# Kernel optimization log

Measured on AMD Instinct MI355X. Metric: run time of the kernel, lower is better.

## Reference

```python
import jax, jax.numpy as jnp
import numpy as np
import math

D_INPUT = 1024
D_Q = 1024
D_K = 1024
D_V = 1024
D_MODEL = 1024
B, S = 4, 2048


def setup_inputs() -> dict:
    key = jax.random.key(0)
    ks = jax.random.split(key, 9)
    sc = 0.02
    return {
        "x": jax.random.normal(ks[0], (B, S, D_INPUT), dtype=jnp.float32),
        "wq": jax.random.normal(ks[1], (D_INPUT, D_Q), dtype=jnp.float32) * sc,
        "bq": jnp.zeros((D_Q,), dtype=jnp.float32),
        "wk": jax.random.normal(ks[2], (D_INPUT, D_K), dtype=jnp.float32) * sc,
        "bk": jnp.zeros((D_K,), dtype=jnp.float32),
        "wv": jax.random.normal(ks[3], (D_INPUT, D_V), dtype=jnp.float32) * sc,
        "bv": jnp.zeros((D_V,), dtype=jnp.float32),
        "wp": jax.random.normal(ks[4], (D_V, D_MODEL), dtype=jnp.float32) * sc,
        "bp": jnp.zeros((D_MODEL,), dtype=jnp.float32),
    }


def reference(x, wq, bq, wk, bk, wv, bv, wp, bp):
    scale = math.sqrt(D_K)  # NOTE: original MULTIPLIES by sqrt(d_k)
    q = x @ wq + bq  # [B,S,Dq]
    k = x @ wk + bk  # [B,S,Dk]
    v = x @ wv + bv  # [B,S,Dv]
    scores = jnp.einsum('bsd,btd->bst', q, k) * scale
    p_attn = jax.nn.softmax(scores, axis=-1)
    # dropout: inference mode (training=False) -> identity
    context = jnp.einsum('bst,btd->bsd', p_attn, v)
    output = context @ wp + bp
    return (output, p_attn)
```

## Files before the change

kernel.cpp:

```cpp
#include <hip/hip_runtime.h>

typedef unsigned short u16;
typedef short bf16x8 __attribute__((ext_vector_type(8)));
typedef float floatx4 __attribute__((ext_vector_type(4)));

static __device__ __forceinline__ u16 f2bf(float f) {
  unsigned int u = __float_as_uint(f);
  unsigned int lsb = (u >> 16) & 1u;
  u += 0x7FFFu + lsb;
  return (u16)(u >> 16);
}
static __device__ __forceinline__ float bf2f(u16 u) {
  return __uint_as_float(((unsigned int)u) << 16);
}

static __device__ __forceinline__ void gl_lds16(const u16* g, u16* l) {
  __builtin_amdgcn_global_load_lds(
      (const __attribute__((address_space(1))) void*)g,
      (__attribute__((address_space(3))) void*)l, 16, 0, 0);
}

__global__ __launch_bounds__(256)
void prep_all(const float* __restrict__ wq, const float* __restrict__ wk,
              const float* __restrict__ wv, const float* __restrict__ wp,
              const float* __restrict__ bq, const float* __restrict__ bk,
              const float* __restrict__ x,
              u16* __restrict__ qkThi, u16* __restrict__ qkTlo,
              u16* __restrict__ wvThi, u16* __restrict__ wpThi,
              float* __restrict__ bqk,
              u16* __restrict__ xhi, u16* __restrict__ xlo,
              u16* __restrict__ xThi) {
  __shared__ float t[32][33];
  const int z = blockIdx.z;
  const int tid = threadIdx.x;
  const int lr = tid >> 3;
  const int lc = (tid & 7) * 4;

  if (z == 4) {
    if (blockIdx.y == 0 && blockIdx.x < 8) {
      const int i = blockIdx.x * 256 + tid;
      bqk[i] = (i < 1024) ? bq[i] : bk[i - 1024];
    }
    return;
  }

  if (z >= 5) {
    const int r0 = ((z - 5) * 32 + blockIdx.y) * 32;
    const int c0 = blockIdx.x * 32;
    float4 v = *(const float4*)(x + (size_t)(r0 + lr) * 1024 + c0 + lc);
    float f[4] = {v.x, v.y, v.z, v.w};
    t[lr][lc + 0] = v.x; t[lr][lc + 1] = v.y; t[lr][lc + 2] = v.z; t[lr][lc + 3] = v.w;
    u16 ph[4], pl[4];
#pragma unroll
    for (int j = 0; j < 4; j++) {
      ph[j] = f2bf(f[j]);
      pl[j] = f2bf(f[j] - bf2f(ph[j]));
    }
    const size_t o = (size_t)(r0 + lr) * 1024 + c0 + lc;
    *(uint2*)(xhi + o) = *(uint2*)ph;
    *(uint2*)(xlo + o) = *(uint2*)pl;
    __syncthreads();
    u16 pt[4];
#pragma unroll
    for (int j = 0; j < 4; j++) pt[j] = f2bf(t[lc + j][lr]);
    const int b = r0 >> 11, rt = r0 & 2047;
    *(uint2*)(xThi + (size_t)b * (1024 * 2048) + (size_t)(c0 + lr) * 2048 + rt + lc) =
        *(uint2*)pt;
    return;
  }

  const float* in = (z == 0) ? wq : (z == 1) ? wk : (z == 2) ? wv : wp;
  u16* hi = (z == 2) ? wvThi : (z == 3) ? wpThi : (qkThi + (size_t)z * 1024 * 1024);
  u16* lo = (z == 0) ? qkTlo : (z == 1) ? (qkTlo + 1024 * 1024) : (u16*)nullptr;
  const int want_lo = (z < 2);

  const int r0 = blockIdx.y * 32, c0 = blockIdx.x * 32;
  float4 v = *(const float4*)(in + (size_t)(r0 + lr) * 1024 + c0 + lc);
  t[lr][lc + 0] = v.x; t[lr][lc + 1] = v.y; t[lr][lc + 2] = v.z; t[lr][lc + 3] = v.w;
  __syncthreads();
  u16 ph[4], pl[4];
#pragma unroll
  for (int j = 0; j < 4; j++) {
    float f = t[lc + j][lr];
    ph[j] = f2bf(f);
    if (want_lo) pl[j] = f2bf(f - bf2f(ph[j]));
  }
  const size_t o = (size_t)(c0 + lr) * 1024 + r0 + lc;
  *(uint2*)(hi + o) = *(uint2*)ph;
  if (want_lo) *(uint2*)(lo + o) = *(uint2*)pl;
}

template<int BM, int SPLIT, int OM, int HB>
__global__ __launch_bounds__(512, 2)
void gemm8(const u16* __restrict__ Ahi, const u16* __restrict__ Alo,
           const u16* __restrict__ Bhi, const u16* __restrict__ Blo,
           const float* __restrict__ bias,
           void* __restrict__ C0, void* __restrict__ C1,
           void* __restrict__ C2, void* __restrict__ C3,
           int lda, int ldb, int ldc, int NP,
           long long aB, long long bB, long long cB, float scale) {
  constexpr int AF = BM / 32;
  constexpr int ASLOT = BM * 32;
  constexpr int L = 2 + BM / 128;
  __shared__ __align__(16) u16 As[4 * ASLOT];
  __shared__ __align__(16) u16 Bs[4 * 8192];

  const int gx = gridDim.x, gy = gridDim.y, gz = gridDim.z;
  const int flat = blockIdx.x + gx * (blockIdx.y + gy * blockIdx.z);
  const int nwg = gx * gy * gz;
  const int lg = (flat & 7) * (nwg >> 3) + (flat >> 3);
  const int bx = lg % gx;
  const int by = (lg / gx) % gy;
  const int bz = lg / (gx * gy);

  const int m0 = by * BM, n0 = bx * 256;
  const u16* pAhi = Ahi + (size_t)bz * aB;
  const u16* pAlo = SPLIT ? (Alo + (size_t)bz * aB) : (const u16*)nullptr;
  const u16* pBhi = Bhi + (size_t)bz * bB;
  const u16* pBlo = SPLIT ? (Blo + (size_t)bz * bB) : (const u16*)nullptr;

  const int tid = threadIdx.x;
  const int w = tid >> 6;
  const int L64 = tid & 63;
  const int rr = L64 & 15, quad = L64 >> 4;
  const int wm = (w >> 2) * (BM / 2);
  const int wn = (w & 3) * 64;

  const int rbase = w * 16 + (L64 >> 2);
  const int coff = (((L64 & 3) ^ ((L64 >> 3) & 3)) << 3);
  const size_t arow = (size_t)(m0 + rbase) * lda + coff;
  const size_t brow = (size_t)(n0 + rbase) * ldb + coff;
  u16* const ldA = As + w * 512;
  u16* const ldB = Bs + w * 512;

  const int aoff = ((wm + rr) << 5) + ((quad ^ ((rr >> 1) & 3)) << 3);
  const int boff = ((wn + rr) << 5) + ((quad ^ ((rr >> 1) & 3)) << 3);

  auto stageA = [&](int H) {
    const u16* src;
    int koff;
    if (SPLIT) {
      const int kt = H >> 1;
      src = (kt < 32) ? pAhi : pAlo;
      koff = ((kt & 15) << 6) + ((H & 1) << 5);
    } else {
      src = pAhi;
      koff = H << 5;
    }
    const u16* g = src + arow + koff;
    u16* l = ldA + (H & 3) * ASLOT;
    gl_lds16(g, l);
    if (BM == 256) gl_lds16(g + (size_t)128 * lda, l + 4096);
  };
  auto stageB = [&](int H) {
    const u16* src;
    int koff;
    if (SPLIT) {
      const int kt = H >> 1;
      src = (kt < 16) ? pBhi : (kt < 32) ? pBlo : pBhi;
      koff = ((kt & 15) << 6) + ((H & 1) << 5);
    } else {
      src = pBhi;
      koff = H << 5;
    }
    const u16* g = src + brow + koff;
    u16* l = ldB + (H & 3) * 8192;
    gl_lds16(g, l);
    gl_lds16(g + (size_t)128 * ldb, l + 4096);
  };

  floatx4 acc[AF][4] = {};
  bf16x8 aE[AF], aO[AF], b01E[2], b01O[2], b23[2];

#define RD_SET(slot, A_, B_)                                                   \
  {                                                                            \
    const u16* ab_ = As + ((slot) & 3) * ASLOT + aoff;                         \
    const u16* bb_ = Bs + ((slot) & 3) * 8192 + boff;                          \
    _Pragma("unroll")                                                          \
    for (int i = 0; i < AF; i++) A_[i] = *(const bf16x8*)(ab_ + i * 512);      \
    B_[0] = *(const bf16x8*)(bb_);                                             \
    B_[1] = *(const bf16x8*)(bb_ + 512);                                       \
  }

#define PAIRX(H, AC, B01C, AN, B01N, STG, RDN, VM)                             \
  {                                                                            \
    __builtin_amdgcn_sched_barrier(0);                                         \
                                                        \
    {                                                                          \
      const u16* bb_ = Bs + ((H) & 3) * 8192 + boff;                           \
      b23[0] = *(const bf16x8*)(bb_ + 1024);                                   \
      b23[1] = *(const bf16x8*)(bb_ + 1536);                                   \
    }                                                                          \
    __builtin_amdgcn_sched_barrier(0);                                         \
                                                            \
    __builtin_amdgcn_s_setprio(1);                                             \
    _Pragma("unroll")                                                          \
    for (int i = 0; i < AF; i++) {                                             \
      acc[i][0] = __builtin_amdgcn_mfma_f32_16x16x32_bf16(AC[i], B01C[0], acc[i][0], 0, 0, 0); \
      acc[i][1] = __builtin_amdgcn_mfma_f32_16x16x32_bf16(AC[i], B01C[1], acc[i][1], 0, 0, 0); \
    }                                                                          \
    __builtin_amdgcn_s_setprio(0);                                             \
    __builtin_amdgcn_sched_barrier(0);                                         \
                               \
    if ((VM) == 4) asm volatile("s_waitcnt vmcnt(4)");                         \
    else if ((VM) == 3) asm volatile("s_waitcnt vmcnt(3)");                    \
    else if ((VM) == 0) asm volatile("s_waitcnt vmcnt(0)");                    \
    __builtin_amdgcn_s_barrier();                                              \
                                \
    if (RDN) RD_SET((H) + 1, AN, B01N);                                        \
    if (STG) { stageA((H) + 3); stageB((H) + 3); }                             \
    __builtin_amdgcn_sched_barrier(0);                                         \
                                                            \
    __builtin_amdgcn_s_setprio(1);                                             \
    _Pragma("unroll")                                                          \
    for (int i = 0; i < AF; i++) {                                             \
      acc[i][2] = __builtin_amdgcn_mfma_f32_16x16x32_bf16(AC[i], b23[0], acc[i][2], 0, 0, 0); \
      acc[i][3] = __builtin_amdgcn_mfma_f32_16x16x32_bf16(AC[i], b23[1], acc[i][3], 0, 0, 0); \
    }                                                                          \
    __builtin_amdgcn_s_setprio(0);                                             \
  }

  stageA(0); stageB(0); stageA(1); stageB(1); stageA(2); stageB(2);
  if (L == 4) asm volatile("s_waitcnt vmcnt(8)");
  else        asm volatile("s_waitcnt vmcnt(6)");
  __builtin_amdgcn_s_barrier();
  RD_SET(0, aE, b01E);

  for (int H = 0; H + 4 < NP; H += 2) {
    PAIRX(H,     aE, b01E, aO, b01O, true, true, L);
    PAIRX(H + 1, aO, b01O, aE, b01E, true, true, L);
  }
  {
    const int T = NP - 4;
    PAIRX(T,     aE, b01E, aO, b01O, true,  true,  L);
    PAIRX(T + 1, aO, b01O, aE, b01E, false, true,  L);
    PAIRX(T + 2, aE, b01E, aO, b01O, false, true,  0);
    PAIRX(T + 3, aO, b01O, aE, b01E, false, false, -1);
  }
#undef PAIRX
#undef RD_SET

#pragma unroll
  for (int i = 0; i < AF; i++) {
    const int mb = m0 + wm + i * 16 + quad * 4;
#pragma unroll
    for (int j = 0; j < 4; j++) {
      const int col = n0 + wn + j * 16 + rr;
      float bvs = 0.f;
      if (HB) bvs = bias[col];
      if (OM == 5) {
        u16* hi; u16* lo;
        if (col < 1024) { hi = (u16*)C0; lo = (u16*)C1; }
        else            { hi = (u16*)C2; lo = (u16*)C3; }
        const int cc = col & 1023;
#pragma unroll
        for (int ii = 0; ii < 4; ii++) {
          const float v = acc[i][j][ii] + bvs;
          const size_t idx = (size_t)(mb + ii) * 1024 + cc;
          const u16 h = f2bf(v);
          hi[idx] = h;
          lo[idx] = f2bf(v - bf2f(h));
        }
      } else if (OM == 0) {
        u16* Cb = (u16*)C0 + (size_t)bz * cB;
#pragma unroll
        for (int ii = 0; ii < 4; ii++) {
          const float v = acc[i][j][ii] * scale + bvs;
          Cb[(size_t)(mb + ii) * ldc + col] = f2bf(v);
        }
      } else {
        float* Cf = (float*)C0 + (size_t)bz * cB;
#pragma unroll
        for (int ii = 0; ii < 4; ii++)
          Cf[(size_t)(mb + ii) * ldc + col] = acc[i][j][ii] * scale + bvs;
      }
    }
  }
}

__global__ __launch_bounds__(256)
void softmax_rows(float* __restrict__ S, u16* __restrict__ Pb) {
  const int row = blockIdx.x;
  float* s = S + (size_t)row * 2048;
  const int tid = threadIdx.x;
  const int w = tid >> 6;
  __shared__ float redm[4];
  __shared__ float reds[4];

  float v[8];
  float mx = -1e30f;
#pragma unroll
  for (int i = 0; i < 8; i++) {
    v[i] = s[tid + 256 * i];
    mx = fmaxf(mx, v[i]);
  }
#pragma unroll
  for (int o = 32; o > 0; o >>= 1) mx = fmaxf(mx, __shfl_xor(mx, o, 64));
  if ((tid & 63) == 0) redm[w] = mx;
  __syncthreads();
  mx = fmaxf(fmaxf(redm[0], redm[1]), fmaxf(redm[2], redm[3]));

  float sum = 0.f;
#pragma unroll
  for (int i = 0; i < 8; i++) {
    v[i] = __expf(v[i] - mx);
    sum += v[i];
  }
#pragma unroll
  for (int o = 32; o > 0; o >>= 1) sum += __shfl_xor(sum, o, 64);
  if ((tid & 63) == 0) reds[w] = sum;
  __syncthreads();
  sum = reds[0] + reds[1] + reds[2] + reds[3];
  const float rs = 1.0f / sum;
#pragma unroll
  for (int i = 0; i < 8; i++) {
    const float p = v[i] * rs;
    s[tid + 256 * i] = p;
    Pb[(size_t)row * 2048 + tid + 256 * i] = f2bf(p);
  }
}

extern "C" void kernel_launch(void* const* d_in, const int* in_sizes, int n_in,
                              void* d_out, int out_size, void* d_ws, size_t ws_size,
                              hipStream_t stream) {
  const float* x  = (const float*)d_in[0];
  const float* wq = (const float*)d_in[1];
  const float* bq = (const float*)d_in[2];
  const float* wk = (const float*)d_in[3];
  const float* bk = (const float*)d_in[4];
  const float* wv = (const float*)d_in[5];
  const float* bv = (const float*)d_in[6];
  const float* wp = (const float*)d_in[7];
  const float* bp = (const float*)d_in[8];

  const size_t MB = 1024 * 1024;
  char* ws = (char*)d_ws;
  u16* qkThi = (u16*)(ws + 0 * MB);
  u16* qkTlo = (u16*)(ws + 4 * MB);
  u16* wvThi = (u16*)(ws + 8 * MB);
  u16* wpThi = (u16*)(ws + 10 * MB);
  float* bqk = (float*)(ws + 12 * MB);
  u16* xhi   = (u16*)(ws + 13 * MB);
  u16* xlo   = (u16*)(ws + 29 * MB);
  u16* qhi   = (u16*)(ws + 45 * MB);
  u16* qlo   = (u16*)(ws + 61 * MB);
  u16* khi   = (u16*)(ws + 77 * MB);
  u16* klo   = (u16*)(ws + 93 * MB);
  u16* xThi  = (u16*)(ws + 109 * MB);
  u16* pbf   = khi;
  u16* px    = qhi;
  u16* ctx   = qlo;

  float* outp = (float*)d_out;
  float* scf  = (float*)d_out + 8388608;

  prep_all<<<dim3(32, 32, 13), dim3(256), 0, stream>>>(
      wq, wk, wv, wp, bq, bk, x, qkThi, qkTlo, wvThi, wpThi, bqk, xhi, xlo, xThi);

  gemm8<256, 1, 5, 1><<<dim3(8, 32, 1), dim3(512), 0, stream>>>(
      xhi, xlo, qkThi, qkTlo, bqk, qhi, qlo, khi, klo,
      1024, 1024, 1024, 96, 0, 0, 0, 1.0f);

  gemm8<256, 1, 2, 0><<<dim3(8, 8, 4), dim3(512), 0, stream>>>(
      qhi, qlo, khi, klo, nullptr, scf, nullptr, nullptr, nullptr,
      1024, 1024, 2048, 96, 2048LL * 1024, 2048LL * 1024, 2048LL * 2048, 32.0f);

  softmax_rows<<<dim3(8192), dim3(256), 0, stream>>>(scf, pbf);

  gemm8<128, 0, 0, 0><<<dim3(4, 16, 4), dim3(512), 0, stream>>>(
      pbf, nullptr, xThi, nullptr, nullptr, px, nullptr, nullptr, nullptr,
      2048, 2048, 1024, 64, 2048LL * 2048, 1024LL * 2048, 2048LL * 1024, 1.0f);

  gemm8<128, 0, 0, 1><<<dim3(4, 64, 1), dim3(512), 0, stream>>>(
      px, nullptr, wvThi, nullptr, bv, ctx, nullptr, nullptr, nullptr,
      1024, 1024, 1024, 32, 0, 0, 0, 1.0f);

  gemm8<128, 0, 2, 1><<<dim3(4, 64, 1), dim3(512), 0, stream>>>(
      ctx, nullptr, wpThi, nullptr, bp, outp, nullptr, nullptr, nullptr,
      1024, 1024, 1024, 32, 0, 0, 0, 1.0f);
}
```

Baseline: 458.8 us.

## Fix GEMM tile at 128x256 with triple-buffered LDS and single register set

Removes the BM template so every GEMM uses a 128-row tile, including the split-bf16 QK projection and score GEMMs that previously used 256 rows. LDS staging goes from 4 slots to 3 (modulo-3 indexing), fragment registers drop from even/odd double sets to a single set, and launch bounds rise to 4 blocks per CU. The aim is higher occupancy and lower LDS use. In exchange, the large GEMMs reuse less data per tile and the next fragments are read after the MFMAs rather than overlapped with them.

```diff
diff --git a/kernel.cpp b/kernel.cpp
--- a/kernel.cpp
+++ b/kernel.cpp
@@ -90,8 +90,8 @@
   if (want_lo) *(uint2*)(lo + o) = *(uint2*)pl;
 }
 
-template<int BM, int SPLIT, int OM, int HB>
-__global__ __launch_bounds__(512, 2)
+template<int SPLIT, int OM, int HB>
+__global__ __launch_bounds__(512, 4)
 void gemm8(const u16* __restrict__ Ahi, const u16* __restrict__ Alo,
            const u16* __restrict__ Bhi, const u16* __restrict__ Blo,
            const float* __restrict__ bias,
@@ -99,11 +99,8 @@
            void* __restrict__ C2, void* __restrict__ C3,
            int lda, int ldb, int ldc, int NP,
            long long aB, long long bB, long long cB, float scale) {
-  constexpr int AF = BM / 32;
-  constexpr int ASLOT = BM * 32;
-  constexpr int L = 2 + BM / 128;
-  __shared__ __align__(16) u16 As[4 * ASLOT];
-  __shared__ __align__(16) u16 Bs[4 * 8192];
+  __shared__ __align__(16) u16 As[3 * 4096];
+  __shared__ __align__(16) u16 Bs[3 * 8192];
 
   const int gx = gridDim.x, gy = gridDim.y, gz = gridDim.z;
   const int flat = blockIdx.x + gx * (blockIdx.y + gy * blockIdx.z);
@@ -113,7 +110,7 @@
   const int by = (lg / gx) % gy;
   const int bz = lg / (gx * gy);
 
-  const int m0 = by * BM, n0 = bx * 256;
+  const int m0 = by * 128, n0 = bx * 256;
   const u16* pAhi = Ahi + (size_t)bz * aB;
   const u16* pAlo = SPLIT ? (Alo + (size_t)bz * aB) : (const u16*)nullptr;
   const u16* pBhi = Bhi + (size_t)bz * bB;
@@ -123,7 +120,7 @@
   const int w = tid >> 6;
   const int L64 = tid & 63;
   const int rr = L64 & 15, quad = L64 >> 4;
-  const int wm = (w >> 2) * (BM / 2);
+  const int wm = (w >> 2) * 64;
   const int wn = (w & 3) * 64;
 
   const int rbase = w * 16 + (L64 >> 2);
@@ -147,10 +144,7 @@
       src = pAhi;
       koff = H << 5;
     }
-    const u16* g = src + arow + koff;
-    u16* l = ldA + (H & 3) * ASLOT;
-    gl_lds16(g, l);
-    if (BM == 256) gl_lds16(g + (size_t)128 * lda, l + 4096);
+    gl_lds16(src + arow + koff, ldA + (H % 3) * 4096);
   };
   auto stageB = [&](int H) {
     const u16* src;
@@ -164,30 +158,20 @@
       koff = H << 5;
     }
     const u16* g = src + brow + koff;
-    u16* l = ldB + (H & 3) * 8192;
+    u16* l = ldB + (H % 3) * 8192;
     gl_lds16(g, l);
     gl_lds16(g + (size_t)128 * ldb, l + 4096);
   };
 
-  floatx4 acc[AF][4] = {};
-  bf16x8 aE[AF], aO[AF], b01E[2], b01O[2], b23[2];
-
-#define RD_SET(slot, A_, B_)                                                   \
-  {                                                                            \
-    const u16* ab_ = As + ((slot) & 3) * ASLOT + aoff;                         \
-    const u16* bb_ = Bs + ((slot) & 3) * 8192 + boff;                          \
-    _Pragma("unroll")                                                          \
-    for (int i = 0; i < AF; i++) A_[i] = *(const bf16x8*)(ab_ + i * 512);      \
-    B_[0] = *(const bf16x8*)(bb_);                                             \
-    B_[1] = *(const bf16x8*)(bb_ + 512);                                       \
-  }
-
-#define PAIRX(H, AC, B01C, AN, B01N, STG, RDN, VM)                             \
+  floatx4 acc[4][4] = {};
+  bf16x8 a[4], b01[2], b23[2];
+
+#define PAIRX(H, STG, RDN, VM)                                                 \
   {                                                                            \
     __builtin_amdgcn_sched_barrier(0);                                         \
                                                         \
     {                                                                          \
-      const u16* bb_ = Bs + ((H) & 3) * 8192 + boff;                           \
+      const u16* bb_ = Bs + ((H) % 3) * 8192 + boff;                           \
       b23[0] = *(const bf16x8*)(bb_ + 1024);                                   \
       b23[1] = *(const bf16x8*)(bb_ + 1536);                                   \
     }                                                                          \
@@ -195,53 +179,70 @@
                                                             \
     __builtin_amdgcn_s_setprio(1);                                             \
     _Pragma("unroll")                                                          \
-    for (int i = 0; i < AF; i++) {                                             \
-      acc[i][0] = __builtin_amdgcn_mfma_f32_16x16x32_bf16(AC[i], B01C[0], acc[i][0], 0, 0, 0); \
-      acc[i][1] = __builtin_amdgcn_mfma_f32_16x16x32_bf16(AC[i], B01C[1], acc[i][1], 0, 0, 0); \
+    for (int i = 0; i < 4; i++) {                                              \
+      acc[i][0] = __builtin_amdgcn_mfma_f32_16x16x32_bf16(a[i], b01[0], acc[i][0], 0, 0, 0); \
+      acc[i][1] = __builtin_amdgcn_mfma_f32_16x16x32_bf16(a[i], b01[1], acc[i][1], 0, 0, 0); \
     }                                                                          \
     __builtin_amdgcn_s_setprio(0);                                             \
     __builtin_amdgcn_sched_barrier(0);                                         \
-                               \
-    if ((VM) == 4) asm volatile("s_waitcnt vmcnt(4)");                         \
-    else if ((VM) == 3) asm volatile("s_waitcnt vmcnt(3)");                    \
-    else if ((VM) == 0) asm volatile("s_waitcnt vmcnt(0)");                    \
+                             \
+    asm volatile("s_waitcnt lgkmcnt(0)" ::: "memory");                         \
     __builtin_amdgcn_s_barrier();                                              \
-                                \
-    if (RDN) RD_SET((H) + 1, AN, B01N);                                        \
+    __builtin_amdgcn_sched_barrier(0);                                         \
+                                       \
     if (STG) { stageA((H) + 3); stageB((H) + 3); }                             \
+    __builtin_amdgcn_sched_barrier(0);                                         \
+                          \
+    if ((VM) == 6) asm volatile("s_waitcnt vmcnt(6)" ::: "memory");            \
+    else if ((VM) == 3) asm volatile("s_waitcnt vmcnt(3)" ::: "memory");       \
+    else if ((VM) == 0) asm volatile("s_waitcnt vmcnt(0)" ::: "memory");       \
+    __builtin_amdgcn_sched_barrier(0);                                         \
+                       \
+    if (RDN) {                                                                 \
+      const u16* bb_ = Bs + (((H) + 1) % 3) * 8192 + boff;                     \
+      b01[0] = *(const bf16x8*)(bb_);                                          \
+      b01[1] = *(const bf16x8*)(bb_ + 512);                                    \
+    }                                                                          \
     __builtin_amdgcn_sched_barrier(0);                                         \
                                                             \
     __builtin_amdgcn_s_setprio(1);                                             \
     _Pragma("unroll")                                                          \
-    for (int i = 0; i < AF; i++) {                                             \
-      acc[i][2] = __builtin_amdgcn_mfma_f32_16x16x32_bf16(AC[i], b23[0], acc[i][2], 0, 0, 0); \
-      acc[i][3] = __builtin_amdgcn_mfma_f32_16x16x32_bf16(AC[i], b23[1], acc[i][3], 0, 0, 0); \
+    for (int i = 0; i < 4; i++) {                                              \
+      acc[i][2] = __builtin_amdgcn_mfma_f32_16x16x32_bf16(a[i], b23[0], acc[i][2], 0, 0, 0); \
+      acc[i][3] = __builtin_amdgcn_mfma_f32_16x16x32_bf16(a[i], b23[1], acc[i][3], 0, 0, 0); \
     }                                                                          \
     __builtin_amdgcn_s_setprio(0);                                             \
+    __builtin_amdgcn_sched_barrier(0);                                         \
+                           \
+    if (RDN) {                                                                 \
+      const u16* ab_ = As + (((H) + 1) % 3) * 4096 + aoff;                     \
+      _Pragma("unroll")                                                        \
+      for (int i = 0; i < 4; i++) a[i] = *(const bf16x8*)(ab_ + i * 512);      \
+    }                                                                          \
   }
 
   stageA(0); stageB(0); stageA(1); stageB(1); stageA(2); stageB(2);
-  if (L == 4) asm volatile("s_waitcnt vmcnt(8)");
-  else        asm volatile("s_waitcnt vmcnt(6)");
+  asm volatile("s_waitcnt vmcnt(6)" ::: "memory");
   __builtin_amdgcn_s_barrier();
-  RD_SET(0, aE, b01E);
-
-  for (int H = 0; H + 4 < NP; H += 2) {
-    PAIRX(H,     aE, b01E, aO, b01O, true, true, L);
-    PAIRX(H + 1, aO, b01O, aE, b01E, true, true, L);
-  }
+  __builtin_amdgcn_sched_barrier(0);
   {
-    const int T = NP - 4;
-    PAIRX(T,     aE, b01E, aO, b01O, true,  true,  L);
-    PAIRX(T + 1, aO, b01O, aE, b01E, false, true,  L);
-    PAIRX(T + 2, aE, b01E, aO, b01O, false, true,  0);
-    PAIRX(T + 3, aO, b01O, aE, b01E, false, false, -1);
-  }
+    const u16* bb_ = Bs + boff;
+    b01[0] = *(const bf16x8*)(bb_);
+    b01[1] = *(const bf16x8*)(bb_ + 512);
+    const u16* ab_ = As + aoff;
+#pragma unroll
+    for (int i = 0; i < 4; i++) a[i] = *(const bf16x8*)(ab_ + i * 512);
+  }
+
+  for (int H = 0; H <= NP - 4; ++H)
+    PAIRX(H, true, true, 6);
+  PAIRX(NP - 3, false, true, 3);
+  PAIRX(NP - 2, false, true, 0);
+  PAIRX(NP - 1, false, false, -1);
 #undef PAIRX
-#undef RD_SET
-
-#pragma unroll
-  for (int i = 0; i < AF; i++) {
+
+#pragma unroll
+  for (int i = 0; i < 4; i++) {
     const int mb = m0 + wm + i * 16 + quad * 4;
 #pragma unroll
     for (int j = 0; j < 4; j++) {
@@ -357,25 +358,25 @@
   prep_all<<<dim3(32, 32, 13), dim3(256), 0, stream>>>(
       wq, wk, wv, wp, bq, bk, x, qkThi, qkTlo, wvThi, wpThi, bqk, xhi, xlo, xThi);
 
-  gemm8<256, 1, 5, 1><<<dim3(8, 32, 1), dim3(512), 0, stream>>>(
+  gemm8<1, 5, 1><<<dim3(8, 64, 1), dim3(512), 0, stream>>>(
       xhi, xlo, qkThi, qkTlo, bqk, qhi, qlo, khi, klo,
       1024, 1024, 1024, 96, 0, 0, 0, 1.0f);
 
-  gemm8<256, 1, 2, 0><<<dim3(8, 8, 4), dim3(512), 0, stream>>>(
+  gemm8<1, 2, 0><<<dim3(8, 16, 4), dim3(512), 0, stream>>>(
       qhi, qlo, khi, klo, nullptr, scf, nullptr, nullptr, nullptr,
       1024, 1024, 2048, 96, 2048LL * 1024, 2048LL * 1024, 2048LL * 2048, 32.0f);
 
   softmax_rows<<<dim3(8192), dim3(256), 0, stream>>>(scf, pbf);
 
-  gemm8<128, 0, 0, 0><<<dim3(4, 16, 4), dim3(512), 0, stream>>>(
+  gemm8<0, 0, 0><<<dim3(4, 16, 4), dim3(512), 0, stream>>>(
       pbf, nullptr, xThi, nullptr, nullptr, px, nullptr, nullptr, nullptr,
       2048, 2048, 1024, 64, 2048LL * 2048, 1024LL * 2048, 2048LL * 1024, 1.0f);
 
-  gemm8<128, 0, 0, 1><<<dim3(4, 64, 1), dim3(512), 0, stream>>>(
+  gemm8<0, 0, 1><<<dim3(4, 64, 1), dim3(512), 0, stream>>>(
       px, nullptr, wvThi, nullptr, bv, ctx, nullptr, nullptr, nullptr,
       1024, 1024, 1024, 32, 0, 0, 0, 1.0f);
 
-  gemm8<128, 0, 2, 1><<<dim3(4, 64, 1), dim3(512), 0, stream>>>(
+  gemm8<0, 2, 1><<<dim3(4, 64, 1), dim3(512), 0, stream>>>(
       ctx, nullptr, wpThi, nullptr, bp, outp, nullptr, nullptr, nullptr,
       1024, 1024, 1024, 32, 0, 0, 0, 1.0f);
 }
```

After: 502.4 us. +9.5%, slower.

## Restructure GEMM main loop with asymmetric A/B prefetch and interleaved LDS-read/MFMA scheduling

Applied to the files above, without the earlier changes.

Rewrites the pipelined bf16 MFMA main loop. It now prefetches B two stages ahead and A three stages ahead, and loads all four B fragments into double-buffered registers. The next stage's LDS reads are interleaved with the current stage's MFMAs using sched_group_barrier, which replaces the split two-half MFMA blocks with setprio. The goal is to hide LDS latency behind MFMAs and to need one barrier per stage. This costs more registers for the B fragments, and the tighter vmcnt accounting risks stalls or races if the counts are wrong.

```diff
diff --git a/kernel.cpp b/kernel.cpp
--- a/kernel.cpp
+++ b/kernel.cpp
@@ -101,7 +101,7 @@
            long long aB, long long bB, long long cB, float scale) {
   constexpr int AF = BM / 32;
   constexpr int ASLOT = BM * 32;
-  constexpr int L = 2 + BM / 128;
+  constexpr int VMS = BM / 128;
   __shared__ __align__(16) u16 As[4 * ASLOT];
   __shared__ __align__(16) u16 Bs[4 * 8192];
 
@@ -170,7 +170,9 @@
   };
 
   floatx4 acc[AF][4] = {};
-  bf16x8 aE[AF], aO[AF], b01E[2], b01O[2], b23[2];
+  bf16x8 aE[AF], aO[AF], bE[4], bO[4];
+
+#define SGB(m, n) __builtin_amdgcn_sched_group_barrier(m, n, 0)
 
 #define RD_SET(slot, A_, B_)                                                   \
   {                                                                            \
@@ -178,67 +180,62 @@
     const u16* bb_ = Bs + ((slot) & 3) * 8192 + boff;                          \
     _Pragma("unroll")                                                          \
     for (int i = 0; i < AF; i++) A_[i] = *(const bf16x8*)(ab_ + i * 512);      \
-    B_[0] = *(const bf16x8*)(bb_);                                             \
-    B_[1] = *(const bf16x8*)(bb_ + 512);                                       \
-  }
-
-#define PAIRX(H, AC, B01C, AN, B01N, STG, RDN, VM)                             \
+    _Pragma("unroll")                                                          \
+    for (int j = 0; j < 4; j++) B_[j] = *(const bf16x8*)(bb_ + j * 512);       \
+  }
+
+#define PAIRX(H, AC, BC, AN, BN, SB, SA, RDN, VM)                              \
   {                                                                            \
     __builtin_amdgcn_sched_barrier(0);                                         \
-                                                        \
-    {                                                                          \
-      const u16* bb_ = Bs + ((H) & 3) * 8192 + boff;                           \
-      b23[0] = *(const bf16x8*)(bb_ + 1024);                                   \
-      b23[1] = *(const bf16x8*)(bb_ + 1536);                                   \
+    if (SB) stageB((H) + 2);                                                   \
+    if (SA) stageA((H) + 3);                                                   \
+    __builtin_amdgcn_sched_barrier(0);                                         \
+    if (RDN) RD_SET((H) + 1, AN, BN);                                          \
+    _Pragma("unroll")                                                          \
+    for (int i = 0; i < AF; i++) {                                             \
+      acc[i][0] = __builtin_amdgcn_mfma_f32_16x16x32_bf16(AC[i], BC[0], acc[i][0], 0, 0, 0); \
+      acc[i][1] = __builtin_amdgcn_mfma_f32_16x16x32_bf16(AC[i], BC[1], acc[i][1], 0, 0, 0); \
+      acc[i][2] = __builtin_amdgcn_mfma_f32_16x16x32_bf16(AC[i], BC[2], acc[i][2], 0, 0, 0); \
+      acc[i][3] = __builtin_amdgcn_mfma_f32_16x16x32_bf16(AC[i], BC[3], acc[i][3], 0, 0, 0); \
+    }                                                                          \
+    if (RDN) {                                                                 \
+      if (AF == 8) {                                                           \
+        SGB(0x100, 2); SGB(0x8, 4); SGB(0x100, 2); SGB(0x8, 4);                \
+        SGB(0x100, 2); SGB(0x8, 4); SGB(0x100, 2); SGB(0x8, 4);                \
+        SGB(0x100, 1); SGB(0x8, 4); SGB(0x100, 1); SGB(0x8, 4);                \
+        SGB(0x100, 1); SGB(0x8, 4); SGB(0x100, 1); SGB(0x8, 4);                \
+      } else {                                                                 \
+        SGB(0x100, 1); SGB(0x8, 2); SGB(0x100, 1); SGB(0x8, 2);                \
+        SGB(0x100, 1); SGB(0x8, 2); SGB(0x100, 1); SGB(0x8, 2);                \
+        SGB(0x100, 1); SGB(0x8, 2); SGB(0x100, 1); SGB(0x8, 2);                \
+        SGB(0x100, 1); SGB(0x8, 2); SGB(0x100, 1); SGB(0x8, 2);                \
+      }                                                                        \
     }                                                                          \
     __builtin_amdgcn_sched_barrier(0);                                         \
-                                                            \
-    __builtin_amdgcn_s_setprio(1);                                             \
-    _Pragma("unroll")                                                          \
-    for (int i = 0; i < AF; i++) {                                             \
-      acc[i][0] = __builtin_amdgcn_mfma_f32_16x16x32_bf16(AC[i], B01C[0], acc[i][0], 0, 0, 0); \
-      acc[i][1] = __builtin_amdgcn_mfma_f32_16x16x32_bf16(AC[i], B01C[1], acc[i][1], 0, 0, 0); \
-    }                                                                          \
-    __builtin_amdgcn_s_setprio(0);                                             \
-    __builtin_amdgcn_sched_barrier(0);                                         \
-                               \
-    if ((VM) == 4) asm volatile("s_waitcnt vmcnt(4)");                         \
-    else if ((VM) == 3) asm volatile("s_waitcnt vmcnt(3)");                    \
-    else if ((VM) == 0) asm volatile("s_waitcnt vmcnt(0)");                    \
+    if ((VM) == 2) asm volatile("s_waitcnt vmcnt(2)" ::: "memory");            \
+    else if ((VM) == 1) asm volatile("s_waitcnt vmcnt(1)" ::: "memory");       \
+    else if ((VM) == 0) asm volatile("s_waitcnt vmcnt(0)" ::: "memory");       \
     __builtin_amdgcn_s_barrier();                                              \
-                                \
-    if (RDN) RD_SET((H) + 1, AN, B01N);                                        \
-    if (STG) { stageA((H) + 3); stageB((H) + 3); }                             \
-    __builtin_amdgcn_sched_barrier(0);                                         \
-                                                            \
-    __builtin_amdgcn_s_setprio(1);                                             \
-    _Pragma("unroll")                                                          \
-    for (int i = 0; i < AF; i++) {                                             \
-      acc[i][2] = __builtin_amdgcn_mfma_f32_16x16x32_bf16(AC[i], b23[0], acc[i][2], 0, 0, 0); \
-      acc[i][3] = __builtin_amdgcn_mfma_f32_16x16x32_bf16(AC[i], b23[1], acc[i][3], 0, 0, 0); \
-    }                                                                          \
-    __builtin_amdgcn_s_setprio(0);                                             \
-  }
-
-  stageA(0); stageB(0); stageA(1); stageB(1); stageA(2); stageB(2);
-  if (L == 4) asm volatile("s_waitcnt vmcnt(8)");
-  else        asm volatile("s_waitcnt vmcnt(6)");
+  }
+
+  stageA(0); stageB(0); stageA(1); stageB(1); stageA(2);
+  if (VMS == 2) asm volatile("s_waitcnt vmcnt(2)" ::: "memory");
+  else          asm volatile("s_waitcnt vmcnt(1)" ::: "memory");
   __builtin_amdgcn_s_barrier();
-  RD_SET(0, aE, b01E);
-
-  for (int H = 0; H + 4 < NP; H += 2) {
-    PAIRX(H,     aE, b01E, aO, b01O, true, true, L);
-    PAIRX(H + 1, aO, b01O, aE, b01E, true, true, L);
-  }
-  {
-    const int T = NP - 4;
-    PAIRX(T,     aE, b01E, aO, b01O, true,  true,  L);
-    PAIRX(T + 1, aO, b01O, aE, b01E, false, true,  L);
-    PAIRX(T + 2, aE, b01E, aO, b01O, false, true,  0);
-    PAIRX(T + 3, aO, b01O, aE, b01E, false, false, -1);
-  }
+  __builtin_amdgcn_sched_barrier(0);
+  RD_SET(0, aE, bE);
+
+  for (int H = 0; H + 6 <= NP; H += 2) {
+    PAIRX(H,     aE, bE, aO, bO, true, true, true, VMS);
+    PAIRX(H + 1, aO, bO, aE, bE, true, true, true, VMS);
+  }
+  PAIRX(NP - 4, aE, bE, aO, bO, true,  true,  true,  VMS);
+  PAIRX(NP - 3, aO, bO, aE, bE, true,  false, true,  0);
+  PAIRX(NP - 2, aE, bE, aO, bO, false, false, true,  -1);
+  PAIRX(NP - 1, aO, bO, aE, bE, false, false, false, -1);
 #undef PAIRX
 #undef RD_SET
+#undef SGB
 
 #pragma unroll
   for (int i = 0; i < AF; i++) {
```

After: 487.0 us. 6.1% more time.
